# Optimization experiments

Measured on AMD Instinct MI355X. Metric: run time of the kernel, lower is better.

## Reference

```python
import jax, jax.numpy as jnp
import numpy as np

N_NODES = 50000
N_EDGES = 600000
HIDDEN = 128
HEADS = 4
HEAD_DIM = HIDDEN // HEADS
RBF = 40


def setup_inputs() -> dict:
    key = jax.random.key(0)
    ks = jax.random.split(key, 16)
    def lin(k, fan_in, fan_out):
        return jax.random.normal(k, (fan_in, fan_out), jnp.float32) / np.sqrt(fan_in)
    return {
        "x": jax.random.normal(ks[0], (N_NODES, HIDDEN), jnp.float32),
        "edge_index": jax.random.randint(ks[1], (2, N_EDGES), 0, N_NODES, jnp.int32),
        "edge_attr_rbf": jax.random.normal(ks[2], (N_EDGES, RBF), jnp.float32),
        "is_defect": jax.random.randint(ks[3], (N_NODES,), 0, 2, jnp.int32),
        "Wq": lin(ks[4], HIDDEN, HIDDEN), "bq": jnp.zeros((HIDDEN,), jnp.float32),
        "Wk": lin(ks[5], HIDDEN, HIDDEN), "bk": jnp.zeros((HIDDEN,), jnp.float32),
        "Wv": lin(ks[6], HIDDEN, HIDDEN), "bv": jnp.zeros((HIDDEN,), jnp.float32),
        "Wo": lin(ks[7], HIDDEN, HIDDEN), "bo": jnp.zeros((HIDDEN,), jnp.float32),
        "Wg1": lin(ks[8], RBF, HIDDEN), "bg1": jnp.zeros((HIDDEN,), jnp.float32),
        "Wg2": lin(ks[9], HIDDEN, HEADS), "bg2": jnp.zeros((HEADS,), jnp.float32),
        "defect_bias": jax.random.normal(ks[10], (HEADS, 4), jnp.float32),
    }


def reference(x, edge_index, edge_attr_rbf, is_defect,
              Wq, bq, Wk, bk, Wv, bv, Wo, bo, Wg1, bg1, Wg2, bg2, defect_bias):
    N = x.shape[0]
    Q = (x @ Wq + bq).reshape(N, HEADS, HEAD_DIM)
    K = (x @ Wk + bk).reshape(N, HEADS, HEAD_DIM)
    V = (x @ Wv + bv).reshape(N, HEADS, HEAD_DIM)
    src, dst = edge_index[0], edge_index[1]
    # per-edge attention scores [E, H]
    score = (Q[src] * K[dst]).sum(-1) / np.sqrt(HEAD_DIM)
    geo_bias = jax.nn.silu(edge_attr_rbf @ Wg1 + bg1) @ Wg2 + bg2  # [E, H]
    defect_code = is_defect[src] * 2 + is_defect[dst]  # [E] in {0,1,2,3}
    score = score + geo_bias + defect_bias[:, defect_code].T
    # segment softmax over edges grouped by dst
    smax = jax.ops.segment_max(score, dst, num_segments=N)  # [N, H]
    e = jnp.exp(score - smax[dst])
    denom = jax.ops.segment_sum(e, dst, num_segments=N)  # [N, H]
    alpha = e / denom[dst]
    msg = V[src] * alpha[..., None]  # [E, H, Hd]
    out = jax.ops.segment_sum(msg, dst, num_segments=N).reshape(N, HIDDEN)
    return out @ Wo + bo
```

## Files before the change

### kernel.cpp

```cpp
#include <hip/hip_runtime.h>
#include <math.h>

#define NN 50000
#define NE 600000
#define HID 128
#define NH 4
#define HD 32
#define NRBF 40
#define SCALE 0.17677669529663687f

typedef __attribute__((ext_vector_type(8))) __bf16 bf16x8;
typedef __attribute__((ext_vector_type(4))) __bf16 bf16x4;
typedef __attribute__((ext_vector_type(4))) float f32x4;

#define MFMA16(a, b, c) __builtin_amdgcn_mfma_f32_16x16x32_bf16(a, b, c, 0, 0, 0)

__device__ __forceinline__ void split2(float v, __bf16& h, __bf16& l) {
  h = (__bf16)v;
  l = (__bf16)(v - (float)h);
}

__global__ void k_prepw(const float* __restrict__ W, __bf16* __restrict__ hi,
                        __bf16* __restrict__ lo, int NKS, int KREAL) {
  int slot = blockIdx.x * 256 + threadIdx.x;
  int total = 8 * NKS * 4 * 16;
  if (slot >= total) return;
  int n = slot & 15, kg = (slot >> 4) & 3;
  int tt = slot >> 6;
  int ks = tt % NKS, nt = tt / NKS;
  bf16x8 h8, l8;
#pragma unroll
  for (int j = 0; j < 8; ++j) {
    int k = ks * 32 + kg * 8 + j;
    float v = (k < KREAL) ? W[k * 128 + nt * 16 + n] : 0.f;
    __bf16 h, l;
    split2(v, h, l);
    h8[j] = h;
    l8[j] = l;
  }
  *(bf16x8*)&hi[slot * 8] = h8;
  *(bf16x8*)&lo[slot * 8] = l8;
}

__global__ __launch_bounds__(256) void k_qkv3(
    const float* __restrict__ x,
    const __bf16* __restrict__ qhi, const __bf16* __restrict__ qlo,
    const __bf16* __restrict__ khi, const __bf16* __restrict__ klo,
    const __bf16* __restrict__ vhi, const __bf16* __restrict__ vlo,
    const float* __restrict__ bq, const float* __restrict__ bk,
    const float* __restrict__ bv,
    __bf16* __restrict__ Qb, float* __restrict__ K, __bf16* __restrict__ Vb,
    int M) {
  __shared__ __bf16 Ahi[16384];
  __shared__ __bf16 Alo[16384];
  int t = threadIdx.x;
  int row0 = blockIdx.x * 128;

#pragma unroll
  for (int rep = 0; rep < 16; ++rep) {
    int idx = rep * 256 + t;
    int e = idx >> 5, c = idx & 31;
    int gn = row0 + e;
    float4 a = (gn < M) ? *(const float4*)&x[gn * 128 + c * 4]
                        : make_float4(0.f, 0.f, 0.f, 0.f);
    int mt = e >> 4, m = e & 15, ks = c >> 3, kg = (c >> 1) & 3, half = c & 1;
    int base = ((((mt * 4 + ks) * 4 + kg) * 16) + m) * 8 + half * 4;
    bf16x4 h4, l4;
    __bf16 h, l;
    split2(a.x, h, l); h4[0] = h; l4[0] = l;
    split2(a.y, h, l); h4[1] = h; l4[1] = l;
    split2(a.z, h, l); h4[2] = h; l4[2] = l;
    split2(a.w, h, l); h4[3] = h; l4[3] = l;
    *(bf16x4*)&Ahi[base] = h4;
    *(bf16x4*)&Alo[base] = l4;
  }
  __syncthreads();

  int wave = t >> 6, l = t & 63;
  int lq = l >> 4, ln = l & 15;
  int nt0 = wave * 2;
  const __bf16* whi[3] = {qhi, khi, vhi};
  const __bf16* wlo[3] = {qlo, klo, vlo};
  const float* bias[3] = {bq, bk, bv};
  const f32x4 fz = {0.f, 0.f, 0.f, 0.f};

#pragma unroll
  for (int w = 0; w < 3; ++w) {
    bf16x8 Bh[2][4], Bl[2][4];
#pragma unroll
    for (int ntl = 0; ntl < 2; ++ntl)
#pragma unroll
      for (int ks = 0; ks < 4; ++ks) {
        int bidx = (((nt0 + ntl) * 4 + ks) * 4 + lq) * 16 + ln;
        Bh[ntl][ks] = *(const bf16x8*)&whi[w][bidx * 8];
        Bl[ntl][ks] = *(const bf16x8*)&wlo[w][bidx * 8];
      }
    f32x4 acc[8][2];
#pragma unroll
    for (int mt = 0; mt < 8; ++mt) { acc[mt][0] = fz; acc[mt][1] = fz; }
#pragma unroll
    for (int mt = 0; mt < 8; ++mt)
#pragma unroll
      for (int ks = 0; ks < 4; ++ks) {
        int as = ((((mt * 4 + ks) * 4 + lq) * 16) + ln) * 8;
        bf16x8 ah = *(bf16x8*)&Ahi[as];
        bf16x8 al = *(bf16x8*)&Alo[as];
#pragma unroll
        for (int ntl = 0; ntl < 2; ++ntl) {
          acc[mt][ntl] = MFMA16(ah, Bh[ntl][ks], acc[mt][ntl]);
          acc[mt][ntl] = MFMA16(al, Bh[ntl][ks], acc[mt][ntl]);
          acc[mt][ntl] = MFMA16(ah, Bl[ntl][ks], acc[mt][ntl]);
        }
      }
    int n0 = nt0 * 16 + ln;
    float b0 = bias[w][n0], b1 = bias[w][n0 + 16];
#pragma unroll
    for (int mt = 0; mt < 8; ++mt)
#pragma unroll
      for (int reg = 0; reg < 4; ++reg) {
        int e = row0 + mt * 16 + lq * 4 + reg;
        if (e < M) {
          float v0 = acc[mt][0][reg] + b0;
          float v1 = acc[mt][1][reg] + b1;
          if (w == 1) {
            K[e * 128 + n0] = v0;
            K[e * 128 + n0 + 16] = v1;
          } else {
            __bf16* dst = (w == 0) ? Qb : Vb;
            dst[e * 128 + n0] = (__bf16)v0;
            dst[e * 128 + n0 + 16] = (__bf16)v1;
          }
        }
      }
  }
}

__global__ __launch_bounds__(256) void k_mm128(
    const float* __restrict__ A, const __bf16* __restrict__ whi,
    const __bf16* __restrict__ wlo, const float* __restrict__ bias,
    float* __restrict__ out, int M) {
  __shared__ __bf16 Ahi[16384];
  __shared__ __bf16 Alo[16384];
  int t = threadIdx.x;
  int row0 = blockIdx.x * 128;
#pragma unroll
  for (int rep = 0; rep < 16; ++rep) {
    int idx = rep * 256 + t;
    int e = idx >> 5, c = idx & 31;
    int gn = row0 + e;
    float4 a = (gn < M) ? *(const float4*)&A[gn * 128 + c * 4]
                        : make_float4(0.f, 0.f, 0.f, 0.f);
    int mt = e >> 4, m = e & 15, ks = c >> 3, kg = (c >> 1) & 3, half = c & 1;
    int base = ((((mt * 4 + ks) * 4 + kg) * 16) + m) * 8 + half * 4;
    bf16x4 h4, l4;
    __bf16 h, l;
    split2(a.x, h, l); h4[0] = h; l4[0] = l;
    split2(a.y, h, l); h4[1] = h; l4[1] = l;
    split2(a.z, h, l); h4[2] = h; l4[2] = l;
    split2(a.w, h, l); h4[3] = h; l4[3] = l;
    *(bf16x4*)&Ahi[base] = h4;
    *(bf16x4*)&Alo[base] = l4;
  }
  __syncthreads();

  int wave = t >> 6, l = t & 63;
  int lq = l >> 4, ln = l & 15;
  int nt0 = wave * 2;
  const f32x4 fz = {0.f, 0.f, 0.f, 0.f};
  bf16x8 Bh[2][4], Bl[2][4];
#pragma unroll
  for (int ntl = 0; ntl < 2; ++ntl)
#pragma unroll
    for (int ks = 0; ks < 4; ++ks) {
      int bidx = (((nt0 + ntl) * 4 + ks) * 4 + lq) * 16 + ln;
      Bh[ntl][ks] = *(const bf16x8*)&whi[bidx * 8];
      Bl[ntl][ks] = *(const bf16x8*)&wlo[bidx * 8];
    }
  f32x4 acc[8][2];
#pragma unroll
  for (int mt = 0; mt < 8; ++mt) { acc[mt][0] = fz; acc[mt][1] = fz; }
#pragma unroll
  for (int mt = 0; mt < 8; ++mt)
#pragma unroll
    for (int ks = 0; ks < 4; ++ks) {
      int as = ((((mt * 4 + ks) * 4 + lq) * 16) + ln) * 8;
      bf16x8 ah = *(bf16x8*)&Ahi[as];
      bf16x8 al = *(bf16x8*)&Alo[as];
#pragma unroll
      for (int ntl = 0; ntl < 2; ++ntl) {
        acc[mt][ntl] = MFMA16(ah, Bh[ntl][ks], acc[mt][ntl]);
        acc[mt][ntl] = MFMA16(al, Bh[ntl][ks], acc[mt][ntl]);
        acc[mt][ntl] = MFMA16(ah, Bl[ntl][ks], acc[mt][ntl]);
      }
    }
  int n0 = nt0 * 16 + ln;
  float b0 = bias[n0], b1 = bias[n0 + 16];
#pragma unroll
  for (int mt = 0; mt < 8; ++mt)
#pragma unroll
    for (int reg = 0; reg < 4; ++reg) {
      int e = row0 + mt * 16 + lq * 4 + reg;
      if (e < M) {
        out[e * 128 + n0] = acc[mt][0][reg] + b0;
        out[e * 128 + n0 + 16] = acc[mt][1][reg] + b1;
      }
    }
}

__global__ __launch_bounds__(256) void k_geo_mfma(
    const float* __restrict__ rbf, const __bf16* __restrict__ g1hi,
    const __bf16* __restrict__ g1lo, const float* __restrict__ bg1,
    const float* __restrict__ Wg2, const float* __restrict__ bg2,
    const int* __restrict__ srcv, const int* __restrict__ dstv,
    const int* __restrict__ isd, const float* __restrict__ db,
    float* __restrict__ biasE) {
  __shared__ __bf16 Ahi[8192];
  int t = threadIdx.x;
  int e0 = blockIdx.x * 128;

  bf16x8 zz = {};
#pragma unroll
  for (int z = 0; z < 4; ++z) *(bf16x8*)&Ahi[(z * 256 + t) * 8] = zz;
  __syncthreads();
#pragma unroll
  for (int rep = 0; rep < 5; ++rep) {
    int idx = rep * 256 + t;
    int e = idx / 10, c = idx % 10;
    int ge = e0 + e;
    float4 a = (ge < NE) ? *(const float4*)&rbf[ge * NRBF + c * 4]
                         : make_float4(0.f, 0.f, 0.f, 0.f);
    int k4 = c * 4;
    int mt = e >> 4, m = e & 15, ks = k4 >> 5, kg = (k4 >> 3) & 3,
        half = (k4 >> 2) & 1;
    int base = ((((mt * 2 + ks) * 4 + kg) * 16) + (m ^ kg)) * 8 + half * 4;
    bf16x4 h4;
    h4[0] = (__bf16)a.x;
    h4[1] = (__bf16)a.y;
    h4[2] = (__bf16)a.z;
    h4[3] = (__bf16)a.w;
    *(bf16x4*)&Ahi[base] = h4;
  }
  __syncthreads();

  int wave = t >> 6, l = t & 63;
  int lq = l >> 4, ln = l & 15;
  int mtb = wave * 2;
  const f32x4 fz = {0.f, 0.f, 0.f, 0.f};
  f32x4 acc[2][8];
#pragma unroll
  for (int mtl = 0; mtl < 2; ++mtl)
#pragma unroll
    for (int nt = 0; nt < 8; ++nt) acc[mtl][nt] = fz;

#pragma unroll
  for (int ks = 0; ks < 2; ++ks) {
    bf16x8 ah[2];
#pragma unroll
    for (int mtl = 0; mtl < 2; ++mtl) {
      int as = (((((mtb + mtl) * 2 + ks) * 4 + lq) * 16) + (ln ^ lq)) * 8;
      ah[mtl] = *(bf16x8*)&Ahi[as];
    }
#pragma unroll
    for (int nt = 0; nt < 8; ++nt) {
      int bidx = ((nt * 2 + ks) * 4 + lq) * 16 + ln;
      bf16x8 bh = *(const bf16x8*)&g1hi[bidx * 8];
      bf16x8 bl = *(const bf16x8*)&g1lo[bidx * 8];
#pragma unroll
      for (int mtl = 0; mtl < 2; ++mtl) {
        acc[mtl][nt] = MFMA16(ah[mtl], bh, acc[mtl][nt]);
        acc[mtl][nt] = MFMA16(ah[mtl], bl, acc[mtl][nt]);
      }
    }
  }

  float p[2][4][4];
#pragma unroll
  for (int mtl = 0; mtl < 2; ++mtl)
#pragma unroll
    for (int reg = 0; reg < 4; ++reg)
#pragma unroll
      for (int hh = 0; hh < 4; ++hh) p[mtl][reg][hh] = 0.f;
#pragma unroll
  for (int nt = 0; nt < 8; ++nt) {
    int n = nt * 16 + ln;
    float b1v = bg1[n];
    float4 w2 = *(const float4*)&Wg2[n * 4];
#pragma unroll
    for (int mtl = 0; mtl < 2; ++mtl)
#pragma unroll
      for (int reg = 0; reg < 4; ++reg) {
        float h = acc[mtl][nt][reg] + b1v;
        float s = h / (1.f + __expf(-h));
        p[mtl][reg][0] = fmaf(s, w2.x, p[mtl][reg][0]);
        p[mtl][reg][1] = fmaf(s, w2.y, p[mtl][reg][1]);
        p[mtl][reg][2] = fmaf(s, w2.z, p[mtl][reg][2]);
        p[mtl][reg][3] = fmaf(s, w2.w, p[mtl][reg][3]);
      }
  }
#pragma unroll
  for (int off = 1; off < 16; off <<= 1)
#pragma unroll
    for (int mtl = 0; mtl < 2; ++mtl)
#pragma unroll
      for (int reg = 0; reg < 4; ++reg)
#pragma unroll
        for (int hh = 0; hh < 4; ++hh)
          p[mtl][reg][hh] += __shfl_xor(p[mtl][reg][hh], off, 64);
#pragma unroll
  for (int mtl = 0; mtl < 2; ++mtl) {
    float v = 0.f;
#pragma unroll
    for (int reg = 0; reg < 4; ++reg)
#pragma unroll
      for (int hh = 0; hh < 4; ++hh)
        if (ln == reg * 4 + hh) v = p[mtl][reg][hh];
    int reg = ln >> 2, hh = ln & 3;
    int e = e0 + (mtb + mtl) * 16 + lq * 4 + reg;
    if (e < NE) {
      int code = isd[srcv[e]] * 2 + isd[dstv[e]];
      biasE[e * 4 + hh] = v + bg2[hh] + db[hh * 4 + code];
    }
  }
}

__global__ void k_count(const int* __restrict__ dstv, int* __restrict__ cnt) {
  int e = blockIdx.x * 256 + threadIdx.x;
  if (e < NE) atomicAdd(&cnt[dstv[e]], 1);
}

__global__ void k_scan1(const int* __restrict__ cnt, int* __restrict__ bsum) {
  __shared__ int sd[256];
  int t = threadIdx.x;
  int i = blockIdx.x * 256 + t;
  sd[t] = (i < NN) ? cnt[i] : 0;
  __syncthreads();
  for (int off = 128; off > 0; off >>= 1) {
    if (t < off) sd[t] += sd[t + off];
    __syncthreads();
  }
  if (t == 0) bsum[blockIdx.x] = sd[0];
}

__global__ void k_scan2(const int* __restrict__ bsum, int* __restrict__ bpre,
                        int* __restrict__ offsets, int nb) {
  __shared__ int sd[256];
  int t = threadIdx.x;
  int v = (t < nb) ? bsum[t] : 0;
  sd[t] = v;
  __syncthreads();
  for (int off = 1; off < 256; off <<= 1) {
    int x = (t >= off) ? sd[t - off] : 0;
    __syncthreads();
    sd[t] += x;
    __syncthreads();
  }
  if (t < nb) bpre[t] = sd[t] - v;
  if (t == 255) offsets[NN] = sd[255];
}

__global__ void k_scan3(const int* __restrict__ cnt, const int* __restrict__ bpre,
                        int* __restrict__ offsets, int* __restrict__ cursor) {
  __shared__ int sd[256];
  int t = threadIdx.x;
  int i = blockIdx.x * 256 + t;
  int v = (i < NN) ? cnt[i] : 0;
  sd[t] = v;
  __syncthreads();
  for (int off = 1; off < 256; off <<= 1) {
    int x = (t >= off) ? sd[t - off] : 0;
    __syncthreads();
    sd[t] += x;
    __syncthreads();
  }
  int excl = sd[t] - v + bpre[blockIdx.x];
  if (i < NN) { offsets[i] = excl; cursor[i] = excl; }
}

__global__ void k_scatter(const int* __restrict__ srcv,
                          const int* __restrict__ dstv,
                          int* __restrict__ cursor,
                          int* __restrict__ eids, int* __restrict__ srcCSR) {
  int e = blockIdx.x * 256 + threadIdx.x;
  if (e < NE) {
    int d = dstv[e];
    int pos = atomicAdd(&cursor[d], 1);
    eids[pos] = e;
    srcCSR[pos] = srcv[e];
  }
}

__global__ __launch_bounds__(128) void k_agg_fused(
    const int* __restrict__ srcCSR, const int* __restrict__ eids,
    const int* __restrict__ offsets, const float* __restrict__ biasE,
    const __bf16* __restrict__ Qb, const float* __restrict__ K,
    const __bf16* __restrict__ Vb, float* __restrict__ accum) {
  int b = blockIdx.x;
  int t = threadIdx.x;
  int h = t >> 5;
  int beg = offsets[b], end = offsets[b + 1];
  float kv = K[b * HID + t];

  float m = -3.0e38f, den = 0.f, acc = 0.f;
  int s_n = (beg < end) ? srcCSR[beg] : 0;
  int e_n = (beg < end) ? eids[beg] : 0;
  for (int i = beg; i < end; ++i) {
    int s = s_n, e = e_n;
    if (i + 1 < end) {
      s_n = srcCSR[i + 1];
      e_n = eids[i + 1];
    }
    float qv = (float)Qb[s * HID + t];
    float vv = (float)Vb[s * HID + t];
    float bias = biasE[e * 4 + h];
    float prod = qv * kv;
#pragma unroll
    for (int off = 1; off < 32; off <<= 1)
      prod += __shfl_xor(prod, off, 32);
    float sc = fmaf(prod, SCALE, bias);
    float mn = fmaxf(m, sc);
    float r = __expf(m - mn);
    float w = __expf(sc - mn);
    den = fmaf(den, r, w);
    acc = fmaf(acc, r, w * vv);
    m = mn;
  }
  accum[b * HID + t] = (end > beg) ? (acc / den) : 0.f;
}

extern "C" void kernel_launch(void* const* d_in, const int* in_sizes, int n_in,
                              void* d_out, int out_size, void* d_ws, size_t ws_size,
                              hipStream_t stream) {
  const float* x = (const float*)d_in[0];
  const int* ei = (const int*)d_in[1];
  const float* rbf = (const float*)d_in[2];
  const int* isd = (const int*)d_in[3];
  const float* Wq = (const float*)d_in[4];
  const float* bq = (const float*)d_in[5];
  const float* Wk = (const float*)d_in[6];
  const float* bk = (const float*)d_in[7];
  const float* Wv = (const float*)d_in[8];
  const float* bv = (const float*)d_in[9];
  const float* Wo = (const float*)d_in[10];
  const float* bo = (const float*)d_in[11];
  const float* Wg1 = (const float*)d_in[12];
  const float* bg1 = (const float*)d_in[13];
  const float* Wg2 = (const float*)d_in[14];
  const float* bg2 = (const float*)d_in[15];
  const float* db = (const float*)d_in[16];
  const int* srcv = ei;
  const int* dstv = ei + NE;

  char* p = (char*)d_ws;
  auto alloc = [&](size_t bytes) {
    void* r = (void*)p;
    p += (bytes + 255) & ~(size_t)255;
    return r;
  };
  __bf16* Qb = (__bf16*)alloc((size_t)NN * HID * 2);
  float* Kb = (float*)alloc((size_t)NN * HID * 4);
  __bf16* Vb = (__bf16*)alloc((size_t)NN * HID * 2);
  float* biasE = (float*)alloc((size_t)NE * NH * 4);
  float* accum = (float*)alloc((size_t)NN * HID * 4);
  int* cnt = (int*)alloc((size_t)NN * 4);
  int* offsets = (int*)alloc((size_t)(NN + 1) * 4);
  int* cursor = (int*)alloc((size_t)NN * 4);
  int* eids = (int*)alloc((size_t)NE * 4);
  int* srcCSR = (int*)alloc((size_t)NE * 4);
  int* bsum = (int*)alloc(256 * 4);
  int* bpre = (int*)alloc(256 * 4);
  __bf16* qhi = (__bf16*)alloc(2048 * 8 * 2);
  __bf16* qlo = (__bf16*)alloc(2048 * 8 * 2);
  __bf16* khi = (__bf16*)alloc(2048 * 8 * 2);
  __bf16* klo = (__bf16*)alloc(2048 * 8 * 2);
  __bf16* vhi = (__bf16*)alloc(2048 * 8 * 2);
  __bf16* vlo = (__bf16*)alloc(2048 * 8 * 2);
  __bf16* ohi = (__bf16*)alloc(2048 * 8 * 2);
  __bf16* olo = (__bf16*)alloc(2048 * 8 * 2);
  __bf16* g1hi = (__bf16*)alloc(1024 * 8 * 2);
  __bf16* g1lo = (__bf16*)alloc(1024 * 8 * 2);

  hipMemsetAsync(cnt, 0, (size_t)NN * 4, stream);

  int gQ = (NN + 127) / 128;
  int gE = (NE + 127) / 128;
  int gEth = (NE + 255) / 256;
  int gS = (NN + 255) / 256;

  k_prepw<<<8, 256, 0, stream>>>(Wq, qhi, qlo, 4, 128);
  k_prepw<<<8, 256, 0, stream>>>(Wk, khi, klo, 4, 128);
  k_prepw<<<8, 256, 0, stream>>>(Wv, vhi, vlo, 4, 128);
  k_prepw<<<8, 256, 0, stream>>>(Wo, ohi, olo, 4, 128);
  k_prepw<<<4, 256, 0, stream>>>(Wg1, g1hi, g1lo, 2, NRBF);

  k_qkv3<<<gQ, 256, 0, stream>>>(x, qhi, qlo, khi, klo, vhi, vlo,
                                 bq, bk, bv, Qb, Kb, Vb, NN);
  k_geo_mfma<<<gE, 256, 0, stream>>>(rbf, g1hi, g1lo, bg1, Wg2, bg2,
                                     srcv, dstv, isd, db, biasE);
  k_count<<<gEth, 256, 0, stream>>>(dstv, cnt);
  k_scan1<<<gS, 256, 0, stream>>>(cnt, bsum);
  k_scan2<<<1, 256, 0, stream>>>(bsum, bpre, offsets, gS);
  k_scan3<<<gS, 256, 0, stream>>>(cnt, bpre, offsets, cursor);
  k_scatter<<<gEth, 256, 0, stream>>>(srcv, dstv, cursor, eids, srcCSR);
  k_agg_fused<<<NN, 128, 0, stream>>>(srcCSR, eids, offsets, biasE,
                                      Qb, Kb, Vb, accum);
  k_mm128<<<gQ, 256, 0, stream>>>(accum, ohi, olo, bo, (float*)d_out, NN);
}
```

Before: 488.5 us.

## Fuse weight prep and edge counting, permute bias into CSR, unroll aggregation by four

The five weight-split launches become one kernel, and the degree count is folded into the geo-bias kernel. The scatter now copies each edge's bias into CSR order, so aggregation reads bias contiguously instead of through eids. The aggregation loop processes four edges per step with a batched online-softmax update, which exposes more memory-level parallelism for the Q/V gathers. The cost is an extra biasCSR buffer plus its write and read, and a slightly different floating-point summation order.

After: 436.6 us. 1.12x faster.

```diff
diff --git a/kernel.cpp b/kernel.cpp
--- a/kernel.cpp
+++ b/kernel.cpp
@@ -20,9 +20,25 @@
   l = (__bf16)(v - (float)h);
 }
 
-__global__ void k_prepw(const float* __restrict__ W, __bf16* __restrict__ hi,
-                        __bf16* __restrict__ lo, int NKS, int KREAL) {
-  int slot = blockIdx.x * 256 + threadIdx.x;
+__global__ void k_prepw_all(
+    const float* __restrict__ Wq, const float* __restrict__ Wk,
+    const float* __restrict__ Wv, const float* __restrict__ Wo,
+    const float* __restrict__ Wg1,
+    __bf16* __restrict__ qhi, __bf16* __restrict__ qlo,
+    __bf16* __restrict__ khi, __bf16* __restrict__ klo,
+    __bf16* __restrict__ vhi, __bf16* __restrict__ vlo,
+    __bf16* __restrict__ ohi, __bf16* __restrict__ olo,
+    __bf16* __restrict__ g1hi, __bf16* __restrict__ g1lo) {
+  int bb = blockIdx.x;
+  const float* W;
+  __bf16 *hi, *lo;
+  int NKS, KREAL, base;
+  if (bb < 8)       { W = Wq;  hi = qhi;  lo = qlo;  NKS = 4; KREAL = 128; base = bb; }
+  else if (bb < 16) { W = Wk;  hi = khi;  lo = klo;  NKS = 4; KREAL = 128; base = bb - 8; }
+  else if (bb < 24) { W = Wv;  hi = vhi;  lo = vlo;  NKS = 4; KREAL = 128; base = bb - 16; }
+  else if (bb < 32) { W = Wo;  hi = ohi;  lo = olo;  NKS = 4; KREAL = 128; base = bb - 24; }
+  else              { W = Wg1; hi = g1hi; lo = g1lo; NKS = 2; KREAL = NRBF; base = bb - 32; }
+  int slot = base * 256 + threadIdx.x;
   int total = 8 * NKS * 4 * 16;
   if (slot >= total) return;
   int n = slot & 15, kg = (slot >> 4) & 3;
@@ -213,7 +229,7 @@
     const float* __restrict__ Wg2, const float* __restrict__ bg2,
     const int* __restrict__ srcv, const int* __restrict__ dstv,
     const int* __restrict__ isd, const float* __restrict__ db,
-    float* __restrict__ biasE) {
+    float* __restrict__ biasE, int* __restrict__ cnt) {
   __shared__ __bf16 Ahi[8192];
   int t = threadIdx.x;
   int e0 = blockIdx.x * 128;
@@ -317,15 +333,12 @@
     int reg = ln >> 2, hh = ln & 3;
     int e = e0 + (mtb + mtl) * 16 + lq * 4 + reg;
     if (e < NE) {
-      int code = isd[srcv[e]] * 2 + isd[dstv[e]];
+      int d = dstv[e];
+      int code = isd[srcv[e]] * 2 + isd[d];
       biasE[e * 4 + hh] = v + bg2[hh] + db[hh * 4 + code];
-    }
-  }
-}
-
-__global__ void k_count(const int* __restrict__ dstv, int* __restrict__ cnt) {
-  int e = blockIdx.x * 256 + threadIdx.x;
-  if (e < NE) atomicAdd(&cnt[dstv[e]], 1);
+      if (hh == 0) atomicAdd(&cnt[d], 1);
+    }
+  }
 }
 
 __global__ void k_scan1(const int* __restrict__ cnt, int* __restrict__ bsum) {
@@ -378,22 +391,25 @@
 
 __global__ void k_scatter(const int* __restrict__ srcv,
                           const int* __restrict__ dstv,
+                          const float* __restrict__ biasE,
                           int* __restrict__ cursor,
-                          int* __restrict__ eids, int* __restrict__ srcCSR) {
+                          int* __restrict__ srcCSR,
+                          float* __restrict__ biasCSR) {
   int e = blockIdx.x * 256 + threadIdx.x;
   if (e < NE) {
     int d = dstv[e];
     int pos = atomicAdd(&cursor[d], 1);
-    eids[pos] = e;
     srcCSR[pos] = srcv[e];
+    float4 b4 = *(const float4*)&biasE[e * 4];
+    *(float4*)&biasCSR[pos * 4] = b4;
   }
 }
 
 __global__ __launch_bounds__(128) void k_agg_fused(
-    const int* __restrict__ srcCSR, const int* __restrict__ eids,
-    const int* __restrict__ offsets, const float* __restrict__ biasE,
-    const __bf16* __restrict__ Qb, const float* __restrict__ K,
-    const __bf16* __restrict__ Vb, float* __restrict__ accum) {
+    const int* __restrict__ srcCSR, const int* __restrict__ offsets,
+    const float* __restrict__ biasCSR, const __bf16* __restrict__ Qb,
+    const float* __restrict__ K, const __bf16* __restrict__ Vb,
+    float* __restrict__ accum) {
   int b = blockIdx.x;
   int t = threadIdx.x;
   int h = t >> 5;
@@ -401,21 +417,41 @@
   float kv = K[b * HID + t];
 
   float m = -3.0e38f, den = 0.f, acc = 0.f;
-  int s_n = (beg < end) ? srcCSR[beg] : 0;
-  int e_n = (beg < end) ? eids[beg] : 0;
-  for (int i = beg; i < end; ++i) {
-    int s = s_n, e = e_n;
-    if (i + 1 < end) {
-      s_n = srcCSR[i + 1];
-      e_n = eids[i + 1];
-    }
+  int i = beg;
+  for (; i + 3 < end; i += 4) {
+    int s0 = srcCSR[i], s1 = srcCSR[i + 1], s2 = srcCSR[i + 2], s3 = srcCSR[i + 3];
+    float q0 = (float)Qb[s0 * HID + t], q1 = (float)Qb[s1 * HID + t];
+    float q2 = (float)Qb[s2 * HID + t], q3 = (float)Qb[s3 * HID + t];
+    float v0 = (float)Vb[s0 * HID + t], v1 = (float)Vb[s1 * HID + t];
+    float v2 = (float)Vb[s2 * HID + t], v3 = (float)Vb[s3 * HID + t];
+    float b0 = biasCSR[i * 4 + h], b1 = biasCSR[(i + 1) * 4 + h];
+    float b2 = biasCSR[(i + 2) * 4 + h], b3 = biasCSR[(i + 3) * 4 + h];
+    float p0 = q0 * kv, p1 = q1 * kv, p2 = q2 * kv, p3 = q3 * kv;
+#pragma unroll
+    for (int off = 1; off < 32; off <<= 1) {
+      p0 += __shfl_xor(p0, off, 32);
+      p1 += __shfl_xor(p1, off, 32);
+      p2 += __shfl_xor(p2, off, 32);
+      p3 += __shfl_xor(p3, off, 32);
+    }
+    float sc0 = fmaf(p0, SCALE, b0), sc1 = fmaf(p1, SCALE, b1);
+    float sc2 = fmaf(p2, SCALE, b2), sc3 = fmaf(p3, SCALE, b3);
+    float mn = fmaxf(m, fmaxf(fmaxf(sc0, sc1), fmaxf(sc2, sc3)));
+    float r = __expf(m - mn);
+    float w0 = __expf(sc0 - mn), w1 = __expf(sc1 - mn);
+    float w2 = __expf(sc2 - mn), w3 = __expf(sc3 - mn);
+    den = fmaf(den, r, (w0 + w1) + (w2 + w3));
+    acc = fmaf(acc, r, fmaf(w0, v0, fmaf(w1, v1, fmaf(w2, v2, w3 * v3))));
+    m = mn;
+  }
+  for (; i < end; ++i) {
+    int s = srcCSR[i];
     float qv = (float)Qb[s * HID + t];
     float vv = (float)Vb[s * HID + t];
-    float bias = biasE[e * 4 + h];
+    float bias = biasCSR[i * 4 + h];
     float prod = qv * kv;
 #pragma unroll
-    for (int off = 1; off < 32; off <<= 1)
-      prod += __shfl_xor(prod, off, 32);
+    for (int off = 1; off < 32; off <<= 1) prod += __shfl_xor(prod, off, 32);
     float sc = fmaf(prod, SCALE, bias);
     float mn = fmaxf(m, sc);
     float r = __expf(m - mn);
@@ -460,11 +496,11 @@
   float* Kb = (float*)alloc((size_t)NN * HID * 4);
   __bf16* Vb = (__bf16*)alloc((size_t)NN * HID * 2);
   float* biasE = (float*)alloc((size_t)NE * NH * 4);
+  float* biasCSR = (float*)alloc((size_t)NE * NH * 4);
   float* accum = (float*)alloc((size_t)NN * HID * 4);
   int* cnt = (int*)alloc((size_t)NN * 4);
   int* offsets = (int*)alloc((size_t)(NN + 1) * 4);
   int* cursor = (int*)alloc((size_t)NN * 4);
-  int* eids = (int*)alloc((size_t)NE * 4);
   int* srcCSR = (int*)alloc((size_t)NE * 4);
   int* bsum = (int*)alloc(256 * 4);
   int* bpre = (int*)alloc(256 * 4);
@@ -486,22 +522,16 @@
   int gEth = (NE + 255) / 256;
   int gS = (NN + 255) / 256;
 
-  k_prepw<<<8, 256, 0, stream>>>(Wq, qhi, qlo, 4, 128);
-  k_prepw<<<8, 256, 0, stream>>>(Wk, khi, klo, 4, 128);
-  k_prepw<<<8, 256, 0, stream>>>(Wv, vhi, vlo, 4, 128);
-  k_prepw<<<8, 256, 0, stream>>>(Wo, ohi, olo, 4, 128);
-  k_prepw<<<4, 256, 0, stream>>>(Wg1, g1hi, g1lo, 2, NRBF);
-
+  k_prepw_all<<<36, 256, 0, stream>>>(Wq, Wk, Wv, Wo, Wg1, qhi, qlo, khi, klo,
+                                      vhi, vlo, ohi, olo, g1hi, g1lo);
   k_qkv3<<<gQ, 256, 0, stream>>>(x, qhi, qlo, khi, klo, vhi, vlo,
                                  bq, bk, bv, Qb, Kb, Vb, NN);
   k_geo_mfma<<<gE, 256, 0, stream>>>(rbf, g1hi, g1lo, bg1, Wg2, bg2,
-                                     srcv, dstv, isd, db, biasE);
-  k_count<<<gEth, 256, 0, stream>>>(dstv, cnt);
+                                     srcv, dstv, isd, db, biasE, cnt);
   k_scan1<<<gS, 256, 0, stream>>>(cnt, bsum);
   k_scan2<<<1, 256, 0, stream>>>(bsum, bpre, offsets, gS);
   k_scan3<<<gS, 256, 0, stream>>>(cnt, bpre, offsets, cursor);
-  k_scatter<<<gEth, 256, 0, stream>>>(srcv, dstv, cursor, eids, srcCSR);
-  k_agg_fused<<<NN, 128, 0, stream>>>(srcCSR, eids, offsets, biasE,
-                                      Qb, Kb, Vb, accum);
+  k_scatter<<<gEth, 256, 0, stream>>>(srcv, dstv, biasE, cursor, srcCSR, biasCSR);
+  k_agg_fused<<<NN, 128, 0, stream>>>(srcCSR, offsets, biasCSR, Qb, Kb, Vb, accum);
   k_mm128<<<gQ, 256, 0, stream>>>(accum, ohi, olo, bo, (float*)d_out, NN);
 }
```
